# Kernel optimization log

Hardware: AMD Instinct MI355X
Metric: run time of the kernel (lower is better)

## Reference

```python
import jax, jax.numpy as jnp
import numpy as np

H = 2048        # hidden size
NK = 16         # key heads
NV = 32         # value heads
DK = 128        # key head dim
DV = 128        # value head dim
K = 4           # conv kernel size
KEY_DIM = NK * DK      # 2048
VAL_DIM = NV * DV      # 4096
CONV_DIM = 2 * KEY_DIM + VAL_DIM  # 8192 (q,k,v pass through the causal conv)
EPS = 1e-6


def setup_inputs() -> dict:
    key = jax.random.key(0)
    ks = jax.random.split(key, 16)
    d = {}
    d["hidden_states"] = jax.random.normal(ks[0], (1, 1, H), jnp.float32)
    for i in range(4):
        d[f"gated_state_{i}"] = 0.1 * jax.random.normal(ks[1 + i], (1, NV, DV, DK), jnp.float32)
        d[f"conv_state_{i}"] = 0.1 * jax.random.normal(ks[5 + i], (1, K - 1, CONV_DIM), jnp.float32)
    # stacked per-layer parameters (leading dim = 4 layers)
    d["W_qkvz"] = 0.02 * jax.random.normal(ks[9], (4, H, 2 * KEY_DIM + 2 * VAL_DIM), jnp.float32)
    d["W_ba"] = 0.02 * jax.random.normal(ks[10], (4, H, 2 * NV), jnp.float32)
    d["conv_w"] = 0.1 * jax.random.normal(ks[11], (4, CONV_DIM, K), jnp.float32)
    d["dt_bias"] = 0.1 * jax.random.normal(ks[12], (4, NV), jnp.float32)
    d["A_log"] = 0.1 * jax.random.normal(ks[13], (4, NV), jnp.float32)
    d["norm_w"] = jnp.ones((4, DV), jnp.float32)
    d["W_out"] = 0.02 * jax.random.normal(ks[14], (4, VAL_DIM, H), jnp.float32)
    return d


def _layer_step(x, S, C, Wq, Wba, cw, dtb, Alog, nw, Wo):
    """One GatedDeltaNet decode step. x:[1,1,H], S:[1,NV,DV,DK], C:[1,K-1,CONV_DIM]."""
    h = x[0, 0]                                  # [H]
    qkvz = h @ Wq                                # [2*KEY + 2*VAL]
    q, k, v, z = jnp.split(qkvz, [KEY_DIM, 2 * KEY_DIM, 2 * KEY_DIM + VAL_DIM])
    ba = h @ Wba
    b, a = ba[:NV], ba[NV:]

    # causal depthwise conv state update + silu
    mixed = jnp.concatenate([q, k, v])           # [CONV_DIM]
    window = jnp.concatenate([C[0], mixed[None]], axis=0)  # [K, CONV_DIM]
    new_C = window[1:][None]                     # [1, K-1, CONV_DIM]
    conv = jax.nn.silu(jnp.einsum('kc,ck->c', window, cw))

    q, k, v = jnp.split(conv, [KEY_DIM, 2 * KEY_DIM])
    q = q.reshape(NK, DK)
    k = k.reshape(NK, DK)
    v = v.reshape(NV, DV)
    # per-head l2 norm on q, k
    q = q * jax.lax.rsqrt(jnp.sum(q * q, -1, keepdims=True) + EPS)
    k = k * jax.lax.rsqrt(jnp.sum(k * k, -1, keepdims=True) + EPS)
    rep = NV // NK
    q = jnp.repeat(q, rep, axis=0)               # [NV, DK]
    k = jnp.repeat(k, rep, axis=0)

    beta = jax.nn.sigmoid(b)                     # [NV]
    g = -jnp.exp(Alog) * jax.nn.softplus(a + dtb)
    decay = jnp.exp(g)                           # [NV]

    # gated delta-rule state update
    S0 = S[0] * decay[:, None, None]             # [NV, DV, DK]
    kv = jnp.einsum('hvd,hd->hv', S0, k)         # [NV, DV]
    S1 = S0 + jnp.einsum('hv,hd->hvd', (v - kv) * beta[:, None], k)
    o = jnp.einsum('hvd,hd->hv', S1, q) * (DK ** -0.5)  # [NV, DV]

    # gated RMSNorm over DV, gated by silu(z)
    zr = z.reshape(NV, DV)
    o = o * jax.lax.rsqrt(jnp.mean(o * o, -1, keepdims=True) + EPS) * nw
    o = o * jax.nn.silu(zr)

    y = (o.reshape(-1) @ Wo)[None, None]         # [1,1,H]
    return y, S1[None], new_C


def _forward(hidden_states, gated_states, conv_states, W_qkvz, W_ba, conv_w, dt_bias, A_log, norm_w, W_out):
    def step(x, inp):
        S, C, Wq, Wba, cw, dtb, Al, nw, Wo = inp
        y, nS, nC = _layer_step(x, S, C, Wq, Wba, cw, dtb, Al, nw, Wo)
        return y, (nS, nC)

    xf, (nS, nC) = jax.lax.scan(
        step, hidden_states,
        (gated_states, conv_states, W_qkvz, W_ba, conv_w, dt_bias, A_log, norm_w, W_out))
    return xf, nS, nC


def reference(hidden_states, gated_state_0, conv_state_0, gated_state_1, conv_state_1,
              gated_state_2, conv_state_2, gated_state_3, conv_state_3,
              W_qkvz, W_ba, conv_w, dt_bias, A_log, norm_w, W_out):
    Ss = jnp.stack([gated_state_0, gated_state_1, gated_state_2, gated_state_3])
    Cs = jnp.stack([conv_state_0, conv_state_1, conv_state_2, conv_state_3])
    xf, nS, nC = _forward(hidden_states, Ss, Cs, W_qkvz, W_ba, conv_w, dt_bias, A_log, norm_w, W_out)
    return (xf, nS[0], nC[0], nS[1], nC[1], nS[2], nC[2], nS[3], nC[3])
```

## Files before the change

kernel.cpp:

```cpp
#include <hip/hip_runtime.h>

#define H_DIM 2048
#define NV 32
#define DK 128
#define DV 128
#define KEY_DIM 2048
#define VAL_DIM 4096
#define CONV_DIM 8192
#define QKVZ_DIM 12288
#define NS_ELEMS (NV * DV * DK)
#define NC_ELEMS (3 * CONV_DIM)

__device__ __forceinline__ float silu_f(float x) { return x / (1.f + expf(-x)); }

__global__ __launch_bounds__(256) void k_gemv_qkvz(
    const float* __restrict__ h, const float* __restrict__ Wq,
    const float* __restrict__ Wba, float* __restrict__ qkvz, float* __restrict__ ba)
{
  int bid = blockIdx.x, t = threadIdx.x;
  __shared__ float4 red[256];
  if (bid < 768) {
    int cb = (bid % 48) * 256;
    int rb = (bid / 48) * 128;
    int jj = cb + (t & 63) * 4;
    int i0 = rb + (t >> 6) * 32;
    float4 acc = {0.f, 0.f, 0.f, 0.f};
    const float* wp = Wq + (size_t)i0 * QKVZ_DIM + jj;
#pragma unroll 8
    for (int ii = 0; ii < 32; ++ii) {
      float hv = h[i0 + ii];
      float4 w = *reinterpret_cast<const float4*>(wp + (size_t)ii * QKVZ_DIM);
      acc.x += hv * w.x; acc.y += hv * w.y; acc.z += hv * w.z; acc.w += hv * w.w;
    }
    red[t] = acc;
    __syncthreads();
    if (t < 64) {
      float4 a = red[t], b = red[t + 64], c = red[t + 128], d = red[t + 192];
      float* qp = qkvz + cb + t * 4;
      atomicAdd(qp + 0, a.x + b.x + c.x + d.x);
      atomicAdd(qp + 1, a.y + b.y + c.y + d.y);
      atomicAdd(qp + 2, a.z + b.z + c.z + d.z);
      atomicAdd(qp + 3, a.w + b.w + c.w + d.w);
    }
  } else {
    int rb = (bid - 768) * 128;
    int col = t & 63;
    int i0 = rb + (t >> 6) * 32;
    float acc = 0.f;
#pragma unroll 8
    for (int ii = 0; ii < 32; ++ii)
      acc += h[i0 + ii] * Wba[(size_t)(i0 + ii) * 64 + col];
    red[t].x = acc;
    __syncthreads();
    if (t < 64)
      atomicAdd(ba + t, red[t].x + red[t + 64].x + red[t + 128].x + red[t + 192].x);
  }
}

__global__ __launch_bounds__(256) void k_state(
    const float* __restrict__ S_in, const float* __restrict__ C_in,
    const float* __restrict__ qkvz, const float* __restrict__ ba,
    const float* __restrict__ conv_w, const float* __restrict__ dt_bias,
    const float* __restrict__ A_log,
    float* __restrict__ nS, float* __restrict__ nC,
    float* __restrict__ o_raw, float* __restrict__ o2acc)
{
  int bid = blockIdx.x, t = threadIdx.x;
  if (bid < 128) {
    int hh = bid >> 2, vchunk = bid & 3;
    int kqh = hh >> 1;
    __shared__ float kk[128], qq[128], vv[32], sc[4];
    auto convval = [&](int c) -> float {
      float4 w = *reinterpret_cast<const float4*>(conv_w + (size_t)c * 4);
      float val = C_in[c] * w.x + C_in[CONV_DIM + c] * w.y +
                  C_in[2 * CONV_DIM + c] * w.z + qkvz[c] * w.w;
      return silu_f(val);
    };
    if (t < 128) kk[t] = convval(KEY_DIM + kqh * 128 + t);
    else         qq[t - 128] = convval(kqh * 128 + (t - 128));
    __syncthreads();
    if (t < 64) {
      float v = kk[t] * kk[t] + kk[t + 64] * kk[t + 64];
      for (int m = 32; m; m >>= 1) v += __shfl_xor(v, m, 64);
      if (t == 0) sc[0] = v;
    } else if (t < 128) {
      int u = t - 64;
      float v = qq[u] * qq[u] + qq[u + 64] * qq[u + 64];
      for (int m = 32; m; m >>= 1) v += __shfl_xor(v, m, 64);
      if (u == 0) sc[1] = v;
    } else if (t < 160) {
      vv[t - 128] = convval(2 * KEY_DIM + hh * 128 + vchunk * 32 + (t - 128));
    } else if (t == 160) {
      float b = ba[hh], a = ba[32 + hh];
      float beta = 1.f / (1.f + expf(-b));
      float x = a + dt_bias[hh];
      float sp = (x > 15.f) ? x : log1pf(expf(x));
      sc[2] = beta;
      sc[3] = expf(-expf(A_log[hh]) * sp);
    }
    __syncthreads();
    float rk = rsqrtf(sc[0] + 1e-6f), rq = rsqrtf(sc[1] + 1e-6f);
    float beta = sc[2], decay = sc[3];
    int lane = t & 31;
    int d0 = lane * 4;
    float4 k4 = {kk[d0] * rk, kk[d0 + 1] * rk, kk[d0 + 2] * rk, kk[d0 + 3] * rk};
    float4 q4 = {qq[d0] * rq, qq[d0 + 1] * rq, qq[d0 + 2] * rq, qq[d0 + 3] * rq};
    float o2loc = 0.f;
    for (int p = 0; p < 4; ++p) {
      int vl = p * 8 + (t >> 5);
      int vrow = vchunk * 32 + vl;
      size_t idx = ((size_t)(hh * 128 + vrow) * 128 + d0);
      float4 s = *reinterpret_cast<const float4*>(S_in + idx);
      s.x *= decay; s.y *= decay; s.z *= decay; s.w *= decay;
      float kv = s.x * k4.x + s.y * k4.y + s.z * k4.z + s.w * k4.w;
      for (int m = 16; m; m >>= 1) kv += __shfl_xor(kv, m, 32);
      float dl = (vv[vl] - kv) * beta;
      float4 s1 = {s.x + dl * k4.x, s.y + dl * k4.y, s.z + dl * k4.z, s.w + dl * k4.w};
      *reinterpret_cast<float4*>(nS + idx) = s1;
      float op = s1.x * q4.x + s1.y * q4.y + s1.z * q4.z + s1.w * q4.w;
      for (int m = 16; m; m >>= 1) op += __shfl_xor(op, m, 32);
      if (lane == 0) {
        float o = op * 0.088388347648318447f;
        o_raw[hh * 128 + vrow] = o;
        o2loc += o * o;
      }
    }
    if (lane == 0) atomicAdd(o2acc + hh, o2loc);
  } else {
    int gt = (bid - 128) * 256 + t;
    if (gt < NC_ELEMS / 4) {
      int c4 = gt * 4;
      int row = c4 >> 13;
      int cc = c4 & (CONV_DIM - 1);
      float4 v = (row < 2)
          ? *reinterpret_cast<const float4*>(C_in + (row + 1) * CONV_DIM + cc)
          : *reinterpret_cast<const float4*>(qkvz + cc);
      *reinterpret_cast<float4*>(nC + row * CONV_DIM + cc) = v;
    }
  }
}

__global__ __launch_bounds__(256) void k_gemv_out(
    const float* __restrict__ o_raw, const float* __restrict__ o2acc,
    const float* __restrict__ qkvz, const float* __restrict__ norm_w,
    const float* __restrict__ Wo, float* __restrict__ y)
{
  int bid = blockIdx.x, t = threadIdx.x;
  int cb = (bid & 7) * 256;
  int rb = (bid >> 3) * 128;
  __shared__ float of[128];
  __shared__ float4 red[256];
  if (t < 128) {
    int c = rb + t;
    int hh = c >> 7;
    float rs = rsqrtf(o2acc[hh] * (1.f / 128.f) + 1e-6f);
    float z = qkvz[CONV_DIM + c];
    of[t] = o_raw[c] * rs * norm_w[c & 127] * silu_f(z);
  }
  __syncthreads();
  int jj = cb + (t & 63) * 4;
  int i0 = (t >> 6) * 32;
  float4 acc = {0.f, 0.f, 0.f, 0.f};
  const float* wp = Wo + (size_t)(rb + i0) * H_DIM + jj;
#pragma unroll 8
  for (int ii = 0; ii < 32; ++ii) {
    float ov = of[i0 + ii];
    float4 w = *reinterpret_cast<const float4*>(wp + (size_t)ii * H_DIM);
    acc.x += ov * w.x; acc.y += ov * w.y; acc.z += ov * w.z; acc.w += ov * w.w;
  }
  red[t] = acc;
  __syncthreads();
  if (t < 64) {
    float4 a = red[t], b = red[t + 64], c = red[t + 128], d = red[t + 192];
    float* yp = y + cb + t * 4;
    atomicAdd(yp + 0, a.x + b.x + c.x + d.x);
    atomicAdd(yp + 1, a.y + b.y + c.y + d.y);
    atomicAdd(yp + 2, a.z + b.z + c.z + d.z);
    atomicAdd(yp + 3, a.w + b.w + c.w + d.w);
  }
}

__global__ void k_copy(const float* __restrict__ src, float* __restrict__ dst, int n4) {
  int i = blockIdx.x * 256 + threadIdx.x;
  if (i < n4)
    reinterpret_cast<float4*>(dst)[i] = reinterpret_cast<const float4*>(src)[i];
}

extern "C" void kernel_launch(void* const* d_in, const int* in_sizes, int n_in,
                              void* d_out, int out_size, void* d_ws, size_t ws_size,
                              hipStream_t stream)
{
  const float* hidden  = (const float*)d_in[0];
  const float* Wq_all  = (const float*)d_in[9];
  const float* Wba_all = (const float*)d_in[10];
  const float* cw_all  = (const float*)d_in[11];
  const float* dtb_all = (const float*)d_in[12];
  const float* Al_all  = (const float*)d_in[13];
  const float* nw_all  = (const float*)d_in[14];
  const float* Wo_all  = (const float*)d_in[15];
  float* out = (float*)d_out;
  float* ws  = (float*)d_ws;

  float* qkvz = ws;
  float* ba   = qkvz + 4 * QKVZ_DIM;
  float* o2   = ba + 4 * 64;
  float* yb   = o2 + 4 * 32;
  float* oraw = yb + 4 * 2048;
  size_t zero_floats = 4 * QKVZ_DIM + 4 * 64 + 4 * 32 + 4 * 2048;
  hipMemsetAsync(d_ws, 0, zero_floats * sizeof(float), stream);

  for (int L = 0; L < 4; ++L) {
    const float* h    = (L == 0) ? hidden : (yb + (size_t)(L - 1) * 2048);
    const float* S_in = (const float*)d_in[1 + 2 * L];
    const float* C_in = (const float*)d_in[2 + 2 * L];
    float* nS = out + 2048 + (size_t)L * (NS_ELEMS + NC_ELEMS);
    float* nC = nS + NS_ELEMS;

    k_gemv_qkvz<<<784, 256, 0, stream>>>(
        h, Wq_all + (size_t)L * H_DIM * QKVZ_DIM,
        Wba_all + (size_t)L * H_DIM * 64,
        qkvz + (size_t)L * QKVZ_DIM, ba + L * 64);

    k_state<<<160, 256, 0, stream>>>(
        S_in, C_in, qkvz + (size_t)L * QKVZ_DIM, ba + L * 64,
        cw_all + (size_t)L * CONV_DIM * 4, dtb_all + L * 32, Al_all + L * 32,
        nS, nC, oraw + (size_t)L * 4096, o2 + L * 32);

    k_gemv_out<<<256, 256, 0, stream>>>(
        oraw + (size_t)L * 4096, o2 + L * 32,
        qkvz + (size_t)L * QKVZ_DIM, nw_all + L * 128,
        Wo_all + (size_t)L * VAL_DIM * H_DIM, yb + (size_t)L * 2048);
  }
  k_copy<<<2, 256, 0, stream>>>(yb + 3 * 2048, out, 512);
}
```

Baseline: 172.7 us.

## Replace atomic reductions with partial-sum buffers and nontemporal weight loads

```diff
diff --git a/kernel.cpp b/kernel.cpp
--- a/kernel.cpp
+++ b/kernel.cpp
@@ -10,74 +10,120 @@
 #define QKVZ_DIM 12288
 #define NS_ELEMS (NV * DV * DK)
 #define NC_ELEMS (3 * CONV_DIM)
+#define NPQ 16
+#define NPY 32
+
+typedef float f32x4 __attribute__((ext_vector_type(4)));
 
 __device__ __forceinline__ float silu_f(float x) { return x / (1.f + expf(-x)); }
+__device__ __forceinline__ f32x4 ntload4(const float* p) {
+  return __builtin_nontemporal_load(reinterpret_cast<const f32x4*>(p));
+}
 
 __global__ __launch_bounds__(256) void k_gemv_qkvz(
-    const float* __restrict__ h, const float* __restrict__ Wq,
-    const float* __restrict__ Wba, float* __restrict__ qkvz, float* __restrict__ ba)
+    const float* __restrict__ hsrc, int hparts,
+    const float* __restrict__ Wq, const float* __restrict__ Wba,
+    float* __restrict__ qpart, float* __restrict__ bapart)
 {
   int bid = blockIdx.x, t = threadIdx.x;
-  __shared__ float4 red[256];
+  __shared__ float hs[128];
+  __shared__ f32x4 red[256];
+  int rb = (bid < 768) ? (bid / 48) * 128 : (bid - 768) * 128;
+  if (t < 128) {
+    float s = 0.f;
+    if (hparts == 1) {
+      s = hsrc[rb + t];
+    } else {
+#pragma unroll
+      for (int p = 0; p < NPY; ++p) s += hsrc[p * H_DIM + rb + t];
+    }
+    hs[t] = s;
+  }
+  __syncthreads();
   if (bid < 768) {
+    int p = bid / 48;
     int cb = (bid % 48) * 256;
-    int rb = (bid / 48) * 128;
     int jj = cb + (t & 63) * 4;
-    int i0 = rb + (t >> 6) * 32;
-    float4 acc = {0.f, 0.f, 0.f, 0.f};
-    const float* wp = Wq + (size_t)i0 * QKVZ_DIM + jj;
+    int i0 = (t >> 6) * 32;
+    f32x4 acc = {0.f, 0.f, 0.f, 0.f};
+    const float* wp = Wq + (size_t)(rb + i0) * QKVZ_DIM + jj;
 #pragma unroll 8
     for (int ii = 0; ii < 32; ++ii) {
-      float hv = h[i0 + ii];
-      float4 w = *reinterpret_cast<const float4*>(wp + (size_t)ii * QKVZ_DIM);
-      acc.x += hv * w.x; acc.y += hv * w.y; acc.z += hv * w.z; acc.w += hv * w.w;
+      float hv = hs[i0 + ii];
+      f32x4 w = ntload4(wp + (size_t)ii * QKVZ_DIM);
+      acc += hv * w;
     }
     red[t] = acc;
     __syncthreads();
     if (t < 64) {
-      float4 a = red[t], b = red[t + 64], c = red[t + 128], d = red[t + 192];
-      float* qp = qkvz + cb + t * 4;
-      atomicAdd(qp + 0, a.x + b.x + c.x + d.x);
-      atomicAdd(qp + 1, a.y + b.y + c.y + d.y);
-      atomicAdd(qp + 2, a.z + b.z + c.z + d.z);
-      atomicAdd(qp + 3, a.w + b.w + c.w + d.w);
+      f32x4 o = red[t] + red[t + 64] + red[t + 128] + red[t + 192];
+      *reinterpret_cast<f32x4*>(qpart + (size_t)p * QKVZ_DIM + cb + t * 4) = o;
     }
   } else {
-    int rb = (bid - 768) * 128;
+    int p = bid - 768;
     int col = t & 63;
-    int i0 = rb + (t >> 6) * 32;
+    int i0 = (t >> 6) * 32;
     float acc = 0.f;
 #pragma unroll 8
     for (int ii = 0; ii < 32; ++ii)
-      acc += h[i0 + ii] * Wba[(size_t)(i0 + ii) * 64 + col];
+      acc += hs[i0 + ii] * Wba[(size_t)(rb + i0 + ii) * 64 + col];
     red[t].x = acc;
     __syncthreads();
     if (t < 64)
-      atomicAdd(ba + t, red[t].x + red[t + 64].x + red[t + 128].x + red[t + 192].x);
+      bapart[p * 64 + t] = red[t].x + red[t + 64].x + red[t + 128].x + red[t + 192].x;
   }
 }
 
 __global__ __launch_bounds__(256) void k_state(
     const float* __restrict__ S_in, const float* __restrict__ C_in,
-    const float* __restrict__ qkvz, const float* __restrict__ ba,
+    const float* __restrict__ qpart, const float* __restrict__ bapart,
     const float* __restrict__ conv_w, const float* __restrict__ dt_bias,
     const float* __restrict__ A_log,
     float* __restrict__ nS, float* __restrict__ nC,
-    float* __restrict__ o_raw, float* __restrict__ o2acc)
+    float* __restrict__ o_raw, float* __restrict__ o2part)
 {
   int bid = blockIdx.x, t = threadIdx.x;
   if (bid < 128) {
     int hh = bid >> 2, vchunk = bid & 3;
     int kqh = hh >> 1;
     __shared__ float kk[128], qq[128], vv[32], sc[4];
-    auto convval = [&](int c) -> float {
-      float4 w = *reinterpret_cast<const float4*>(conv_w + (size_t)c * 4);
+    __shared__ float qs[128], ks[128], vs[32], o2s[8];
+    if (t < 128) {
+      float s = 0.f;
+#pragma unroll
+      for (int p = 0; p < NPQ; ++p) s += qpart[(size_t)p * QKVZ_DIM + kqh * 128 + t];
+      qs[t] = s;
+    } else {
+      int u = t - 128;
+      float s = 0.f;
+#pragma unroll
+      for (int p = 0; p < NPQ; ++p) s += qpart[(size_t)p * QKVZ_DIM + KEY_DIM + kqh * 128 + u];
+      ks[u] = s;
+    }
+    if (t < 32) {
+      float s = 0.f;
+#pragma unroll
+      for (int p = 0; p < NPQ; ++p)
+        s += qpart[(size_t)p * QKVZ_DIM + 2 * KEY_DIM + hh * 128 + vchunk * 32 + t];
+      vs[t] = s;
+    }
+    float bval = 0.f, aval = 0.f;
+    if (t == 160) {
+#pragma unroll
+      for (int p = 0; p < NPQ; ++p) {
+        bval += bapart[p * 64 + hh];
+        aval += bapart[p * 64 + 32 + hh];
+      }
+    }
+    __syncthreads();
+    auto convval = [&](int c, float last) -> float {
+      f32x4 w = *reinterpret_cast<const f32x4*>(conv_w + (size_t)c * 4);
       float val = C_in[c] * w.x + C_in[CONV_DIM + c] * w.y +
-                  C_in[2 * CONV_DIM + c] * w.z + qkvz[c] * w.w;
+                  C_in[2 * CONV_DIM + c] * w.z + last * w.w;
       return silu_f(val);
     };
-    if (t < 128) kk[t] = convval(KEY_DIM + kqh * 128 + t);
-    else         qq[t - 128] = convval(kqh * 128 + (t - 128));
+    if (t < 128) kk[t] = convval(KEY_DIM + kqh * 128 + t, ks[t]);
+    else         qq[t - 128] = convval(kqh * 128 + (t - 128), qs[t - 128]);
     __syncthreads();
     if (t < 64) {
       float v = kk[t] * kk[t] + kk[t + 64] * kk[t + 64];
@@ -89,11 +135,10 @@
       for (int m = 32; m; m >>= 1) v += __shfl_xor(v, m, 64);
       if (u == 0) sc[1] = v;
     } else if (t < 160) {
-      vv[t - 128] = convval(2 * KEY_DIM + hh * 128 + vchunk * 32 + (t - 128));
+      vv[t - 128] = convval(2 * KEY_DIM + hh * 128 + vchunk * 32 + (t - 128), vs[t - 128]);
     } else if (t == 160) {
-      float b = ba[hh], a = ba[32 + hh];
-      float beta = 1.f / (1.f + expf(-b));
-      float x = a + dt_bias[hh];
+      float beta = 1.f / (1.f + expf(-bval));
+      float x = aval + dt_bias[hh];
       float sp = (x > 15.f) ? x : log1pf(expf(x));
       sc[2] = beta;
       sc[3] = expf(-expf(A_log[hh]) * sp);
@@ -103,20 +148,20 @@
     float beta = sc[2], decay = sc[3];
     int lane = t & 31;
     int d0 = lane * 4;
-    float4 k4 = {kk[d0] * rk, kk[d0 + 1] * rk, kk[d0 + 2] * rk, kk[d0 + 3] * rk};
-    float4 q4 = {qq[d0] * rq, qq[d0 + 1] * rq, qq[d0 + 2] * rq, qq[d0 + 3] * rq};
+    f32x4 k4 = {kk[d0] * rk, kk[d0 + 1] * rk, kk[d0 + 2] * rk, kk[d0 + 3] * rk};
+    f32x4 q4 = {qq[d0] * rq, qq[d0 + 1] * rq, qq[d0 + 2] * rq, qq[d0 + 3] * rq};
     float o2loc = 0.f;
     for (int p = 0; p < 4; ++p) {
       int vl = p * 8 + (t >> 5);
       int vrow = vchunk * 32 + vl;
       size_t idx = ((size_t)(hh * 128 + vrow) * 128 + d0);
-      float4 s = *reinterpret_cast<const float4*>(S_in + idx);
-      s.x *= decay; s.y *= decay; s.z *= decay; s.w *= decay;
+      f32x4 s = *reinterpret_cast<const f32x4*>(S_in + idx);
+      s *= decay;
       float kv = s.x * k4.x + s.y * k4.y + s.z * k4.z + s.w * k4.w;
       for (int m = 16; m; m >>= 1) kv += __shfl_xor(kv, m, 32);
       float dl = (vv[vl] - kv) * beta;
-      float4 s1 = {s.x + dl * k4.x, s.y + dl * k4.y, s.z + dl * k4.z, s.w + dl * k4.w};
-      *reinterpret_cast<float4*>(nS + idx) = s1;
+      f32x4 s1 = s + dl * k4;
+      *reinterpret_cast<f32x4*>(nS + idx) = s1;
       float op = s1.x * q4.x + s1.y * q4.y + s1.z * q4.z + s1.w * q4.w;
       for (int m = 16; m; m >>= 1) op += __shfl_xor(op, m, 32);
       if (lane == 0) {
@@ -125,65 +170,79 @@
         o2loc += o * o;
       }
     }
-    if (lane == 0) atomicAdd(o2acc + hh, o2loc);
+    if (lane == 0) o2s[t >> 5] = o2loc;
+    __syncthreads();
+    if (t == 0) {
+      float s = 0.f;
+#pragma unroll
+      for (int w = 0; w < 8; ++w) s += o2s[w];
+      o2part[hh * 4 + vchunk] = s;
+    }
   } else {
     int gt = (bid - 128) * 256 + t;
     if (gt < NC_ELEMS / 4) {
       int c4 = gt * 4;
       int row = c4 >> 13;
       int cc = c4 & (CONV_DIM - 1);
-      float4 v = (row < 2)
-          ? *reinterpret_cast<const float4*>(C_in + (row + 1) * CONV_DIM + cc)
-          : *reinterpret_cast<const float4*>(qkvz + cc);
-      *reinterpret_cast<float4*>(nC + row * CONV_DIM + cc) = v;
+      f32x4 v;
+      if (row < 2) {
+        v = *reinterpret_cast<const f32x4*>(C_in + (row + 1) * CONV_DIM + cc);
+      } else {
+        v = (f32x4){0.f, 0.f, 0.f, 0.f};
+#pragma unroll
+        for (int p = 0; p < NPQ; ++p)
+          v += *reinterpret_cast<const f32x4*>(qpart + (size_t)p * QKVZ_DIM + cc);
+      }
+      *reinterpret_cast<f32x4*>(nC + row * CONV_DIM + cc) = v;
     }
   }
 }
 
 __global__ __launch_bounds__(256) void k_gemv_out(
-    const float* __restrict__ o_raw, const float* __restrict__ o2acc,
-    const float* __restrict__ qkvz, const float* __restrict__ norm_w,
-    const float* __restrict__ Wo, float* __restrict__ y)
+    const float* __restrict__ o_raw, const float* __restrict__ o2part,
+    const float* __restrict__ qpart, const float* __restrict__ norm_w,
+    const float* __restrict__ Wo, float* __restrict__ ypart)
 {
   int bid = blockIdx.x, t = threadIdx.x;
   int cb = (bid & 7) * 256;
-  int rb = (bid >> 3) * 128;
+  int hh = bid >> 3;
+  int rb = hh * 128;
   __shared__ float of[128];
-  __shared__ float4 red[256];
+  __shared__ f32x4 red[256];
   if (t < 128) {
-    int c = rb + t;
-    int hh = c >> 7;
-    float rs = rsqrtf(o2acc[hh] * (1.f / 128.f) + 1e-6f);
-    float z = qkvz[CONV_DIM + c];
-    of[t] = o_raw[c] * rs * norm_w[c & 127] * silu_f(z);
+    float o2 = o2part[hh * 4] + o2part[hh * 4 + 1] + o2part[hh * 4 + 2] + o2part[hh * 4 + 3];
+    float rs = rsqrtf(o2 * (1.f / 128.f) + 1e-6f);
+    float z = 0.f;
+#pragma unroll
+    for (int p = 0; p < NPQ; ++p) z += qpart[(size_t)p * QKVZ_DIM + CONV_DIM + rb + t];
+    of[t] = o_raw[rb + t] * rs * norm_w[t] * silu_f(z);
   }
   __syncthreads();
   int jj = cb + (t & 63) * 4;
   int i0 = (t >> 6) * 32;
-  float4 acc = {0.f, 0.f, 0.f, 0.f};
+  f32x4 acc = {0.f, 0.f, 0.f, 0.f};
   const float* wp = Wo + (size_t)(rb + i0) * H_DIM + jj;
 #pragma unroll 8
   for (int ii = 0; ii < 32; ++ii) {
     float ov = of[i0 + ii];
-    float4 w = *reinterpret_cast<const float4*>(wp + (size_t)ii * H_DIM);
-    acc.x += ov * w.x; acc.y += ov * w.y; acc.z += ov * w.z; acc.w += ov * w.w;
+    f32x4 w = ntload4(wp + (size_t)ii * H_DIM);
+    acc += ov * w;
   }
   red[t] = acc;
   __syncthreads();
   if (t < 64) {
-    float4 a = red[t], b = red[t + 64], c = red[t + 128], d = red[t + 192];
-    float* yp = y + cb + t * 4;
-    atomicAdd(yp + 0, a.x + b.x + c.x + d.x);
-    atomicAdd(yp + 1, a.y + b.y + c.y + d.y);
-    atomicAdd(yp + 2, a.z + b.z + c.z + d.z);
-    atomicAdd(yp + 3, a.w + b.w + c.w + d.w);
-  }
-}
-
-__global__ void k_copy(const float* __restrict__ src, float* __restrict__ dst, int n4) {
-  int i = blockIdx.x * 256 + threadIdx.x;
-  if (i < n4)
-    reinterpret_cast<float4*>(dst)[i] = reinterpret_cast<const float4*>(src)[i];
+    f32x4 o = red[t] + red[t + 64] + red[t + 128] + red[t + 192];
+    *reinterpret_cast<f32x4*>(ypart + (size_t)hh * H_DIM + cb + t * 4) = o;
+  }
+}
+
+__global__ __launch_bounds__(256) void k_final(const float* __restrict__ ypart,
+                                               float* __restrict__ dst) {
+  int c = blockIdx.x * 256 + threadIdx.x;
+  float s = 0.f;
+#pragma unroll
+  for (int p = 0; p < NPY; ++p) s += ypart[p * H_DIM + c];
+  dst[c] = s;
 }
 
 extern "C" void kernel_launch(void* const* d_in, const int* in_sizes, int n_in,
@@ -201,35 +260,34 @@
   float* out = (float*)d_out;
   float* ws  = (float*)d_ws;
 
-  float* qkvz = ws;
-  float* ba   = qkvz + 4 * QKVZ_DIM;
-  float* o2   = ba + 4 * 64;
-  float* yb   = o2 + 4 * 32;
-  float* oraw = yb + 4 * 2048;
-  size_t zero_floats = 4 * QKVZ_DIM + 4 * 64 + 4 * 32 + 4 * 2048;
-  hipMemsetAsync(d_ws, 0, zero_floats * sizeof(float), stream);
+  float* qpart  = ws;
+  float* bapart = qpart + NPQ * QKVZ_DIM;
+  float* o2part = bapart + NPQ * 64;
+  float* ypart  = o2part + 128;
+  float* oraw   = ypart + NPY * H_DIM;
 
   for (int L = 0; L < 4; ++L) {
-    const float* h    = (L == 0) ? hidden : (yb + (size_t)(L - 1) * 2048);
+    const float* hsrc = (L == 0) ? hidden : ypart;
+    int hparts        = (L == 0) ? 1 : NPY;
     const float* S_in = (const float*)d_in[1 + 2 * L];
     const float* C_in = (const float*)d_in[2 + 2 * L];
     float* nS = out + 2048 + (size_t)L * (NS_ELEMS + NC_ELEMS);
     float* nC = nS + NS_ELEMS;
 
     k_gemv_qkvz<<<784, 256, 0, stream>>>(
-        h, Wq_all + (size_t)L * H_DIM * QKVZ_DIM,
+        hsrc, hparts,
+        Wq_all + (size_t)L * H_DIM * QKVZ_DIM,
         Wba_all + (size_t)L * H_DIM * 64,
-        qkvz + (size_t)L * QKVZ_DIM, ba + L * 64);
+        qpart, bapart);
 
     k_state<<<160, 256, 0, stream>>>(
-        S_in, C_in, qkvz + (size_t)L * QKVZ_DIM, ba + L * 64,
+        S_in, C_in, qpart, bapart,
         cw_all + (size_t)L * CONV_DIM * 4, dtb_all + L * 32, Al_all + L * 32,
-        nS, nC, oraw + (size_t)L * 4096, o2 + L * 32);
+        nS, nC, oraw, o2part);
 
     k_gemv_out<<<256, 256, 0, stream>>>(
-        oraw + (size_t)L * 4096, o2 + L * 32,
-        qkvz + (size_t)L * QKVZ_DIM, nw_all + L * 128,
-        Wo_all + (size_t)L * VAL_DIM * H_DIM, yb + (size_t)L * 2048);
-  }
-  k_copy<<<2, 256, 0, stream>>>(yb + 3 * 2048, out, 512);
-}
+        oraw, o2part, qpart, nw_all + L * 128,
+        Wo_all + (size_t)L * VAL_DIM * H_DIM, ypart);
+  }
+  k_final<<<8, 256, 0, stream>>>(ypart, out);
+}
```

Result: faster. 141.9 us (-17.8%).
